# Optimization experiments

Hardware: AMD Instinct MI355X
Metric: run time of the kernel (lower is better)

## Reference

```python
import jax, jax.numpy as jnp
import numpy as np

GROUP_IDX = np.array([[(0, 1, 2), (3, 0, 1), (2, 3, 0), (1, 2, 3)][g % 4] for g in range(20)])
PAULI_Z = np.array([1.0, -1.0], dtype=np.float32)
RAND_WIRES = [3, 1, 0, 2]  # frozen structure standing in for qml.RandomLayers(seed=42)


def apply_1q(state, U, w):
    # state: (2,2,2,2) complex, U: (2,2)
    s = jnp.tensordot(U, state, axes=([1], [w]))
    return jnp.moveaxis(s, 0, w)


def apply_cnot(state, c, t):
    s = jnp.moveaxis(state, (c, t), (0, 1))
    s = s.at[1].set(s[1, ::-1])  # flip target where control == 1
    return jnp.moveaxis(s, (0, 1), (c, t))


def rot_mat(phi, theta, omega):
    # qml.Rot = RZ(phi) -> RY(theta) -> RZ(omega)
    c, s = jnp.cos(theta / 2), jnp.sin(theta / 2)
    ep = jnp.exp(-0.5j * (phi + omega))
    em = jnp.exp(0.5j * (phi - omega))
    return jnp.stack([jnp.stack([ep * c, -em * s]), jnp.stack([jnp.conj(em) * s, jnp.conj(ep) * c])])


def rx_mat(t):
    c, s = jnp.cos(t / 2), jnp.sin(t / 2)
    return jnp.stack([jnp.stack([c + 0j, -1j * s]), jnp.stack([-1j * s, c + 0j])])


def ry_mat(t):
    c, s = jnp.cos(t / 2), jnp.sin(t / 2)
    return jnp.stack([jnp.stack([c + 0j, -s + 0j]), jnp.stack([s + 0j, c + 0j])])


def rz_mat(t):
    e0, e1 = jnp.exp(-0.5j * t), jnp.exp(0.5j * t)
    z = jnp.zeros_like(e0)
    return jnp.stack([jnp.stack([e0, z]), jnp.stack([z, e1])])


def circuit(patch, rand_params):
    # patch: (4,) pixels of one 2x2 block
    angles = patch[GROUP_IDX] * np.pi  # (20, 3): (phi, theta, omega) per group
    state = jnp.zeros((2, 2, 2, 2), jnp.complex64).at[0, 0, 0, 0].set(1.0)

    def step(state, abc):
        U = rot_mat(abc[0], abc[1], abc[2])
        for j in range(4):
            state = apply_1q(state, U, j)
            for k in range(3):
                state = apply_cnot(state, k, k + 1)
            state = apply_cnot(state, 3, 0)
        return state, None

    state, _ = jax.lax.scan(step, state, angles)
    # deterministic stand-in for RandomLayers(rand_params)
    p = rand_params.reshape(-1)
    mats = [rx_mat, ry_mat, rz_mat, rx_mat]
    for i in range(4):
        state = apply_1q(state, mats[i](p[i]), RAND_WIRES[i])
        if i == 1:
            state = apply_cnot(state, 0, 2)
        if i == 3:
            state = apply_cnot(state, 1, 3)
    probs = jnp.real(state * jnp.conj(state))  # (2,2,2,2)
    z = jnp.asarray(PAULI_Z)
    ev = [jnp.sum(probs * z.reshape([2 if a == j else 1 for a in range(4)])) for j in range(4)]
    return jnp.stack(ev)  # (4,) PauliZ expvals


def setup_inputs() -> dict:
    key = jax.random.key(0)
    k1, k2, k3, k4 = jax.random.split(key, 4)
    images = jax.random.uniform(k1, (64, 1, 28, 28), dtype=jnp.float32)
    rand_params = jax.random.uniform(k2, (1, 4), dtype=jnp.float32, maxval=2.0 * np.pi)
    fc_w = jax.random.normal(k3, (10, 784), dtype=jnp.float32) * 0.05
    fc_b = jax.random.normal(k4, (10,), dtype=jnp.float32) * 0.05
    return {"images": images, "rand_params": rand_params, "fc_w": fc_w, "fc_b": fc_b}


def reference(images, rand_params, fc_w, fc_b):
    b = images.shape[0]
    # 2x2 non-overlapping patches, order [p(j,k), p(j,k+1), p(j+1,k), p(j+1,k+1)]
    patches = images[:, 0].reshape(b, 14, 2, 14, 2).transpose(0, 1, 3, 2, 4).reshape(b, 196, 4)
    q = jax.vmap(jax.vmap(circuit, in_axes=(0, None)), in_axes=(0, None))(patches, rand_params)
    logits = q.reshape(b, -1) @ fc_w.T + fc_b  # (b, 10)
    return jax.nn.log_softmax(logits, axis=1)
```

## Files before the change

### kernel.cpp

```cpp
#include <hip/hip_runtime.h>
#include <math.h>

#define PI_F 3.14159265358979323846f


struct Gates { int xm[84]; int sm[84]; int fin[4]; };

constexpr Gates make_gates() {
  Gates gt{};
  int F[4] = {1, 2, 4, 8};
  int H[4] = {1, 2, 4, 8};
  int ng = 0;
  auto cnot = [&](int c, int t) {
    const int pc = 3 - c, pt = 3 - t;
    F[pt] ^= F[pc];
    for (int p = 0; p < 4; ++p)
      if (H[p] & (1 << pt)) H[p] ^= (1 << pc);
  };
  auto gate = [&](int w) {
    const int p = 3 - w;
    int m = 0;
    for (int q = 0; q < 4; ++q)
      if (H[q] & (1 << p)) m |= 1 << q;
    gt.xm[ng] = m; gt.sm[ng] = F[p]; ++ng;
  };
  for (int step = 0; step < 20; ++step)
    for (int j = 0; j < 4; ++j) {
      gate(j);
      cnot(0, 1); cnot(1, 2); cnot(2, 3); cnot(3, 0);
    }
  gate(3); gate(1); cnot(0, 2); gate(0); gate(2); cnot(1, 3);
  for (int p = 0; p < 4; ++p) gt.fin[p] = F[p];
  return gt;
}

constexpr Gates GT = make_gates();

template <int CTRL>
__device__ __forceinline__ float dppmov(float v) {
  return __int_as_float(
      __builtin_amdgcn_mov_dpp(__float_as_int(v), CTRL, 0xF, 0xF, true));
}

template <int M>
__device__ __forceinline__ float sxor(float v) {
  if constexpr (M == 0) return v;
  else if constexpr (M == 9 || M == 10 || M == 11) return __shfl_xor(v, M);
  else if constexpr ((M & 8) != 0) return sxor<M ^ 15>(dppmov<0x140>(v));
  else if constexpr ((M & 4) != 0) return sxor<M ^ 7>(dppmov<0x141>(v));
  else if constexpr (M == 1) return dppmov<0xB1>(v);
  else if constexpr (M == 2) return dppmov<0x4E>(v);
  else return dppmov<0x1B>(v);
}

template <int XM, int SM>
__device__ __forceinline__ void apply_gate(float& re, float& im, unsigned P,
                                           float WR, float WI, float XR, float XI) {
  const float pre = sxor<XM>(re);
  const float pim = sxor<XM>(im);
  const unsigned sb = ((P >> SM) & 1u) << 31;
  const float cmi = __uint_as_float(__float_as_uint(WI) ^ sb);
  const float cpr = __uint_as_float(__float_as_uint(XR) ^ sb);
  const float nre = WR * re - cmi * im + cpr * pre - XI * pim;
  const float nim = WR * im + cmi * re + cpr * pim + XI * pre;
  re = nre; im = nim;
}

template <int K>
struct Loop80 {
  static __device__ __forceinline__ void run(float& re, float& im, unsigned P,
      const float (&wr)[4], const float (&wi)[4],
      const float (&xr)[4], const float (&xi)[4]) {
    constexpr int g = (K >> 2) & 3;
    apply_gate<GT.xm[K], GT.sm[K]>(re, im, P, wr[g], wi[g], xr[g], xi[g]);
    Loop80<K + 1>::run(re, im, P, wr, wi, xr, xi);
  }
};
template <>
struct Loop80<80> {
  static __device__ __forceinline__ void run(float&, float&, unsigned,
      const float (&)[4], const float (&)[4],
      const float (&)[4], const float (&)[4]) {}
};

__global__ __launch_bounds__(256) void qcnn_circuit_kernel(
    const float* __restrict__ images,
    const float* __restrict__ rp,
    float* __restrict__ qout)
{
  const int gtid = blockIdx.x * 256 + threadIdx.x;
  const int c    = gtid >> 4;
  const int l16  = gtid & 15;

  const int b  = c / 196;
  const int pi = c - b * 196;
  const int pj = pi / 14;
  const int pk = pi - pj * 14;

  const float* img = images + b * 784 + (2 * pj) * 28 + 2 * pk;
  const float2 r0 = *reinterpret_cast<const float2*>(img);
  const float2 r1 = *reinterpret_cast<const float2*>(img + 28);
  float px[4];
  px[0] = r0.x * PI_F;
  px[1] = r0.y * PI_F;
  px[2] = r1.x * PI_F;
  px[3] = r1.y * PI_F;

  unsigned P = 0;
  if (l16 & 1) P ^= 0xAAAAu;
  if (l16 & 2) P ^= 0xCCCCu;
  if (l16 & 4) P ^= 0xF0F0u;
  if (l16 & 8) P ^= 0xFF00u;

  float wr[4], wi[4], xr[4], xi[4];
  {
    const int GIphi[4] = {0, 3, 2, 1};
    const int GIth [4] = {1, 0, 3, 2};
    const int GIom [4] = {2, 1, 0, 3};
#pragma unroll
    for (int g = 0; g < 4; ++g) {
      const float phi = px[GIphi[g]], th = px[GIth[g]], om = px[GIom[g]];
      const float a = 0.5f * (phi + om), d = 0.5f * (phi - om), h = 0.5f * th;
      const float sa = __sinf(a), ca = __cosf(a);
      const float sd = __sinf(d), cd = __cosf(d);
      const float st = __sinf(h), ct = __cosf(h);
      wr[g] =  ca * ct;  wi[g] = -sa * ct;
      xr[g] = -cd * st;  xi[g] = -sd * st;
    }
  }

  float re = (l16 == 0) ? 1.f : 0.f;
  float im = 0.f;

  Loop80<0>::run(re, im, P, wr, wi, xr, xi);

  {
    const float s0 = __sinf(0.5f * rp[0]), c0 = __cosf(0.5f * rp[0]);
    apply_gate<GT.xm[80], GT.sm[80]>(re, im, P, c0, 0.f, 0.f, -s0);
    const float s1 = __sinf(0.5f * rp[1]), c1 = __cosf(0.5f * rp[1]);
    apply_gate<GT.xm[81], GT.sm[81]>(re, im, P, c1, 0.f, -s1, 0.f);
    const float s2 = __sinf(0.5f * rp[2]), c2 = __cosf(0.5f * rp[2]);
    apply_gate<GT.xm[82], GT.sm[82]>(re, im, P, c2, -s2, 0.f, 0.f);
    const float s3 = __sinf(0.5f * rp[3]), c3 = __cosf(0.5f * rp[3]);
    apply_gate<GT.xm[83], GT.sm[83]>(re, im, P, c3, 0.f, 0.f, -s3);
  }

  const float pr = re * re + im * im;
  float e0 = __uint_as_float(__float_as_uint(pr) ^ (((P >> GT.fin[3]) & 1u) << 31));
  float e1 = __uint_as_float(__float_as_uint(pr) ^ (((P >> GT.fin[2]) & 1u) << 31));
  float e2 = __uint_as_float(__float_as_uint(pr) ^ (((P >> GT.fin[1]) & 1u) << 31));
  float e3 = __uint_as_float(__float_as_uint(pr) ^ (((P >> GT.fin[0]) & 1u) << 31));
#pragma unroll
  for (int q = 0; q < 1; ++q) {
    e0 += dppmov<0xB1>(e0); e0 += dppmov<0x4E>(e0); e0 += dppmov<0x141>(e0); e0 += dppmov<0x140>(e0);
    e1 += dppmov<0xB1>(e1); e1 += dppmov<0x4E>(e1); e1 += dppmov<0x141>(e1); e1 += dppmov<0x140>(e1);
    e2 += dppmov<0xB1>(e2); e2 += dppmov<0x4E>(e2); e2 += dppmov<0x141>(e2); e2 += dppmov<0x140>(e2);
    e3 += dppmov<0xB1>(e3); e3 += dppmov<0x4E>(e3); e3 += dppmov<0x141>(e3); e3 += dppmov<0x140>(e3);
  }
  float v = e0;
  v = (l16 == 1) ? e1 : v;
  v = (l16 == 2) ? e2 : v;
  v = (l16 == 3) ? e3 : v;
  if (l16 < 4) qout[c * 4 + l16] = v;
}

__global__ __launch_bounds__(64) void qcnn_fc_kernel(
    const float* __restrict__ q,
    const float* __restrict__ fcw,
    const float* __restrict__ fcb,
    float* __restrict__ out)
{
  const int b    = blockIdx.x;
  const int lane = threadIdx.x;
  const float4* q4 = reinterpret_cast<const float4*>(q + b * 784);
  const float4* w4 = reinterpret_cast<const float4*>(fcw);

  float acc[10];
#pragma unroll
  for (int o = 0; o < 10; ++o) acc[o] = 0.f;

  for (int i = lane; i < 196; i += 64) {
    const float4 qv = q4[i];
#pragma unroll
    for (int o = 0; o < 10; ++o) {
      const float4 wv = w4[o * 196 + i];
      acc[o] += qv.x * wv.x + qv.y * wv.y + qv.z * wv.z + qv.w * wv.w;
    }
  }

#pragma unroll
  for (int o = 0; o < 10; ++o) {
    for (int off = 32; off > 0; off >>= 1)
      acc[o] += __shfl_down(acc[o], off);
  }

  if (lane == 0) {
    float logits[10];
    float mx = -1e30f;
#pragma unroll
    for (int o = 0; o < 10; ++o) {
      logits[o] = acc[o] + fcb[o];
      mx = fmaxf(mx, logits[o]);
    }
    float se = 0.f;
#pragma unroll
    for (int o = 0; o < 10; ++o) se += __expf(logits[o] - mx);
    const float lse = mx + __logf(se);
#pragma unroll
    for (int o = 0; o < 10; ++o) out[b * 10 + o] = logits[o] - lse;
  }
}


extern "C" void kernel_launch(void* const* d_in, const int* in_sizes, int n_in,
                              void* d_out, int out_size, void* d_ws, size_t ws_size,
                              hipStream_t stream) {
  const float* images = (const float*)d_in[0];
  const float* rp     = (const float*)d_in[1];
  const float* fcw    = (const float*)d_in[2];
  const float* fcb    = (const float*)d_in[3];
  float* out = (float*)d_out;
  float* q   = (float*)d_ws;

  qcnn_circuit_kernel<<<784, 256, 0, stream>>>(images, rp, q);
  qcnn_fc_kernel<<<64, 64, 0, stream>>>(q, fcw, fcb, out);
}
```

Baseline: 18.32 us.

## Use packed FP32 gate math, smaller circuit blocks, and wider FC reduction

The gate update is rewritten as inline v_pk_mul/v_pk_fma packed-FP32 assembly, so real and imaginary parts are computed together in about four packed ops. The circuit kernel moves to 64-thread blocks with four times as many blocks, which should spread work across more CUs. The FC kernel uses 256 threads, one float4 per thread, with a cross-wave shared-memory reduction and a lane-parallel log-softmax instead of a serial lane-0 loop. The inline asm relies on exact op_sel/neg semantics and may hurt scheduling around the DPP moves.

```diff
diff --git a/kernel.cpp b/kernel.cpp
--- a/kernel.cpp
+++ b/kernel.cpp
@@ -59,11 +59,20 @@
   const float pre = sxor<XM>(re);
   const float pim = sxor<XM>(im);
   const unsigned sb = ((P >> SM) & 1u) << 31;
-  const float cmi = __uint_as_float(__float_as_uint(WI) ^ sb);
-  const float cpr = __uint_as_float(__float_as_uint(XR) ^ sb);
-  const float nre = WR * re - cmi * im + cpr * pre - XI * pim;
-  const float nim = WR * im + cmi * re + cpr * pim + XI * pre;
-  re = nre; im = nim;
+  float2 s;  s.x = re;   s.y = im;
+  float2 p2; p2.x = pre; p2.y = pim;
+  float2 wx; wx.x = WR;  wx.y = XI;
+  float2 cc;
+  cc.x = __uint_as_float(__float_as_uint(WI) ^ sb);
+  cc.y = __uint_as_float(__float_as_uint(XR) ^ sb);
+  float2 d;
+  asm("v_pk_mul_f32 %0, %1, %3 op_sel:[0,0] op_sel_hi:[1,0]\n\t"
+      "v_pk_fma_f32 %0, %1, %4, %0 op_sel:[1,0,0] op_sel_hi:[0,0,1] neg_lo:[0,1,0]\n\t"
+      "v_pk_fma_f32 %0, %2, %4, %0 op_sel:[0,1,0] op_sel_hi:[1,1,1]\n\t"
+      "v_pk_fma_f32 %0, %2, %3, %0 op_sel:[1,1,0] op_sel_hi:[0,1,1] neg_lo:[0,1,0]"
+      : "=&v"(d)
+      : "v"(s), "v"(p2), "v"(wx), "v"(cc));
+  re = d.x; im = d.y;
 }
 
 template <int K>
@@ -83,12 +92,12 @@
       const float (&)[4], const float (&)[4]) {}
 };
 
-__global__ __launch_bounds__(256) void qcnn_circuit_kernel(
+__global__ __launch_bounds__(64) void qcnn_circuit_kernel(
     const float* __restrict__ images,
     const float* __restrict__ rp,
     float* __restrict__ qout)
 {
-  const int gtid = blockIdx.x * 256 + threadIdx.x;
+  const int gtid = blockIdx.x * 64 + threadIdx.x;
   const int c    = gtid >> 4;
   const int l16  = gtid & 15;
 
@@ -150,13 +159,10 @@
   float e1 = __uint_as_float(__float_as_uint(pr) ^ (((P >> GT.fin[2]) & 1u) << 31));
   float e2 = __uint_as_float(__float_as_uint(pr) ^ (((P >> GT.fin[1]) & 1u) << 31));
   float e3 = __uint_as_float(__float_as_uint(pr) ^ (((P >> GT.fin[0]) & 1u) << 31));
-#pragma unroll
-  for (int q = 0; q < 1; ++q) {
-    e0 += dppmov<0xB1>(e0); e0 += dppmov<0x4E>(e0); e0 += dppmov<0x141>(e0); e0 += dppmov<0x140>(e0);
-    e1 += dppmov<0xB1>(e1); e1 += dppmov<0x4E>(e1); e1 += dppmov<0x141>(e1); e1 += dppmov<0x140>(e1);
-    e2 += dppmov<0xB1>(e2); e2 += dppmov<0x4E>(e2); e2 += dppmov<0x141>(e2); e2 += dppmov<0x140>(e2);
-    e3 += dppmov<0xB1>(e3); e3 += dppmov<0x4E>(e3); e3 += dppmov<0x141>(e3); e3 += dppmov<0x140>(e3);
-  }
+  e0 += dppmov<0xB1>(e0); e0 += dppmov<0x4E>(e0); e0 += dppmov<0x141>(e0); e0 += dppmov<0x140>(e0);
+  e1 += dppmov<0xB1>(e1); e1 += dppmov<0x4E>(e1); e1 += dppmov<0x141>(e1); e1 += dppmov<0x140>(e1);
+  e2 += dppmov<0xB1>(e2); e2 += dppmov<0x4E>(e2); e2 += dppmov<0x141>(e2); e2 += dppmov<0x140>(e2);
+  e3 += dppmov<0xB1>(e3); e3 += dppmov<0x4E>(e3); e3 += dppmov<0x141>(e3); e3 += dppmov<0x140>(e3);
   float v = e0;
   v = (l16 == 1) ? e1 : v;
   v = (l16 == 2) ? e2 : v;
@@ -164,50 +170,56 @@
   if (l16 < 4) qout[c * 4 + l16] = v;
 }
 
-__global__ __launch_bounds__(64) void qcnn_fc_kernel(
+__global__ __launch_bounds__(256) void qcnn_fc_kernel(
     const float* __restrict__ q,
     const float* __restrict__ fcw,
     const float* __restrict__ fcb,
     float* __restrict__ out)
 {
-  const int b    = blockIdx.x;
-  const int lane = threadIdx.x;
-  const float4* q4 = reinterpret_cast<const float4*>(q + b * 784);
-  const float4* w4 = reinterpret_cast<const float4*>(fcw);
+  const int b = blockIdx.x;
+  const int t = threadIdx.x;
 
   float acc[10];
 #pragma unroll
   for (int o = 0; o < 10; ++o) acc[o] = 0.f;
 
-  for (int i = lane; i < 196; i += 64) {
-    const float4 qv = q4[i];
+  if (t < 196) {
+    const float4 qv = reinterpret_cast<const float4*>(q + b * 784)[t];
+    const float4* w4 = reinterpret_cast<const float4*>(fcw);
 #pragma unroll
     for (int o = 0; o < 10; ++o) {
-      const float4 wv = w4[o * 196 + i];
+      const float4 wv = w4[o * 196 + t];
       acc[o] += qv.x * wv.x + qv.y * wv.y + qv.z * wv.z + qv.w * wv.w;
     }
   }
 
 #pragma unroll
   for (int o = 0; o < 10; ++o) {
+#pragma unroll
     for (int off = 32; off > 0; off >>= 1)
-      acc[o] += __shfl_down(acc[o], off);
-  }
-
-  if (lane == 0) {
-    float logits[10];
-    float mx = -1e30f;
-#pragma unroll
-    for (int o = 0; o < 10; ++o) {
-      logits[o] = acc[o] + fcb[o];
-      mx = fmaxf(mx, logits[o]);
-    }
-    float se = 0.f;
-#pragma unroll
-    for (int o = 0; o < 10; ++o) se += __expf(logits[o] - mx);
-    const float lse = mx + __logf(se);
-#pragma unroll
-    for (int o = 0; o < 10; ++o) out[b * 10 + o] = logits[o] - lse;
+      acc[o] += __shfl_xor(acc[o], off);
+  }
+
+  __shared__ float ws[4][10];
+  const int wid = t >> 6;
+  if ((t & 63) == 0) {
+#pragma unroll
+    for (int o = 0; o < 10; ++o) ws[wid][o] = acc[o];
+  }
+  __syncthreads();
+
+  if (t < 16) {
+    float lgv = -1e30f;
+    if (t < 10)
+      lgv = ws[0][t] + ws[1][t] + ws[2][t] + ws[3][t] + fcb[t];
+    float mx = lgv;
+#pragma unroll
+    for (int s = 1; s < 16; s <<= 1) mx = fmaxf(mx, __shfl_xor(mx, s));
+    float ex = (t < 10) ? __expf(lgv - mx) : 0.f;
+    float se = ex;
+#pragma unroll
+    for (int s = 1; s < 16; s <<= 1) se += __shfl_xor(se, s);
+    if (t < 10) out[b * 10 + t] = lgv - mx - __logf(se);
   }
 }
 
@@ -222,6 +234,6 @@
   float* out = (float*)d_out;
   float* q   = (float*)d_ws;
 
-  qcnn_circuit_kernel<<<784, 256, 0, stream>>>(images, rp, q);
-  qcnn_fc_kernel<<<64, 64, 0, stream>>>(q, fcw, fcb, out);
-}
+  qcnn_circuit_kernel<<<3136, 64, 0, stream>>>(images, rp, q);
+  qcnn_fc_kernel<<<64, 256, 0, stream>>>(q, fcw, fcb, out);
+}
```

Result: faster. 15.90 us (-13.2%).
